# Optimization experiments

Hardware: AMD Instinct MI355X
Metric: run time of the kernel (lower is better)

Reference implementation:

```python
import jax, jax.numpy as jnp
import numpy as np
from jax import lax

BN_EPS = 1e-5

def setup_inputs() -> dict:
    key = jax.random.key(0)
    k1, k2, k3, k4 = jax.random.split(key, 4)
    B, Cin, Cout, H, Wd = 32, 256, 256, 56, 56
    x = jax.random.normal(k1, (B, Cin, H, Wd), dtype=jnp.float32)
    gate = jax.random.uniform(k2, (B, Cin), dtype=jnp.float32)
    # expert convs: one 3x3 conv per input channel; stacked into a full OIHW kernel
    W = jax.random.normal(k3, (Cout, Cin, 3, 3), dtype=jnp.float32) * (1.0 / np.sqrt(Cin * 9))
    # per-expert bias: expert i contributes gate[:, i] * b_expert[i]
    b_expert = jax.random.normal(k4, (Cin, Cout), dtype=jnp.float32) * 0.01
    gamma = jnp.ones((Cout,), dtype=jnp.float32)
    beta = jnp.zeros((Cout,), dtype=jnp.float32)
    return {"x": x, "gate": gate, "W": W, "b_expert": b_expert, "gamma": gamma, "beta": beta}

def reference(x, gate, W, b_expert, gamma, beta):
    # MoELayer: sum_i gate[:, i] * conv_i(x[:, i:i+1]) == conv2d(x * gate, W_full)
    xg = x * gate[:, :, None, None]
    y = lax.conv_general_dilated(
        xg, W, window_strides=(1, 1), padding=((1, 1), (1, 1)),
        dimension_numbers=("NCHW", "OIHW", "NCHW"))
    bias = jnp.einsum("bi,io->bo", gate, b_expert)  # gate-weighted expert biases
    y = y + bias[:, :, None, None]
    # BatchNorm2d (training mode: batch statistics over N,H,W) + ReLU
    mean = jnp.mean(y, axis=(0, 2, 3))
    var = jnp.var(y, axis=(0, 2, 3))
    inv = lax.rsqrt(var + BN_EPS)
    y = (y - mean[None, :, None, None]) * (inv * gamma)[None, :, None, None] + beta[None, :, None, None]
    return jax.nn.relu(y)
```

## Files before the change

kernel.cpp:

```cpp
#include <hip/hip_runtime.h>
#include <cstdint>
#include <cstddef>

#define S_IMG   3136
#define PPOS    3364
#define PLANE_B (PPOS * 16)
#define XPAD_BYTES (32 * 8 * 4 * PLANE_B)
#define WT2_OFF    XPAD_BYTES
#define WT2_BYTES  (9 * 8 * 4 * 256 * 16)
#define STATS_OFF  (WT2_OFF + WT2_BYTES)

typedef __bf16 bf16x8 __attribute__((ext_vector_type(8)));
typedef short  s16x8  __attribute__((ext_vector_type(8)));
typedef float  f32x4  __attribute__((ext_vector_type(4)));

__device__ __forceinline__ unsigned short f2bf(float f) {
    unsigned u = __float_as_uint(f);
    u += 0x7fffu + ((u >> 16) & 1u);
    return (unsigned short)(u >> 16);
}

__device__ __forceinline__ void gll16(const void* g, void* l) {
    __builtin_amdgcn_global_load_lds(
        (const __attribute__((address_space(1))) void*)g,
        (__attribute__((address_space(3))) void*)l, 16, 0, 0);
}

__global__ __launch_bounds__(256) void prep_small(const float* __restrict__ W,
                                                  const float* __restrict__ gate,
                                                  const float* __restrict__ be,
                                                  char* __restrict__ xpad,
                                                  char* __restrict__ wt2,
                                                  float* __restrict__ stats) {
    const int blk = blockIdx.x;
    if (blk < 917) {
        const int t = blk * 256 + threadIdx.x;
        if (t < 1024 * 228) {
            const int plane = t / 228, pi = t % 228;
            int pos;
            if (pi < 58)       pos = pi;
            else if (pi < 116) pos = 3306 + (pi - 58);
            else { const int q = pi - 116; pos = ((q >> 1) + 1) * 58 + (q & 1) * 57; }
            *(uint4*)(xpad + (size_t)plane * PLANE_B + (size_t)pos * 16) =
                make_uint4(0u, 0u, 0u, 0u);
        } else if (t < 1024 * 228 + 512) {
            stats[t - 1024 * 228] = 0.f;
        }
    } else if (blk < 1205) {
        const int g = (blk - 917) * 256 + threadIdx.x;
        if (g >= 9 * 256 * 32) return;
        const int ci8 = g % 32;
        const int co  = (g / 32) % 256;
        const int tap = g / (32 * 256);
        const float* src = W + ((size_t)co * 256 + ci8 * 8) * 9 + tap;
        unsigned short v[8];
#pragma unroll
        for (int j = 0; j < 8; ++j) v[j] = f2bf(src[j * 9]);
        uint4 o;
        o.x = (unsigned)v[0] | ((unsigned)v[1] << 16);
        o.y = (unsigned)v[2] | ((unsigned)v[3] << 16);
        o.z = (unsigned)v[4] | ((unsigned)v[5] << 16);
        o.w = (unsigned)v[6] | ((unsigned)v[7] << 16);
        *(uint4*)(wt2 + ((size_t)(tap * 32 + ci8) * 256 + co) * 16) = o;
    } else {
        const int b = blk - 1205, co = threadIdx.x;
        const float* gb = gate + b * 256;
        float s = 0.f;
        for (int ci = 0; ci < 256; ++ci) s += gb[ci] * be[ci * 256 + co];
        stats[512 + b * 256 + co] = s;
    }
}

__global__ __launch_bounds__(256) void prep_x(const float* __restrict__ x,
                                              const float* __restrict__ gate,
                                              char* __restrict__ xpad) {
    __shared__ unsigned short xb[14336];
    const int tid = threadIdx.x;
    const int b = blockIdx.x / 56, h = blockIdx.x % 56;
    const float* xbase = x + (size_t)b * 256 * S_IMG + h * 56;
    const float* gb = gate + b * 256;
#pragma unroll
    for (int i = 0; i < 14; ++i) {
        const int e4 = i * 1024 + tid * 4;
        const int ci = e4 / 56, w = e4 % 56;
        const float4 v = *(const float4*)(xbase + (size_t)ci * S_IMG + w);
        const float g = gb[ci];
        ushort4 o;
        o.x = f2bf(v.x * g); o.y = f2bf(v.y * g);
        o.z = f2bf(v.z * g); o.w = f2bf(v.w * g);
        *(ushort4*)(xb + e4) = o;
    }
    __syncthreads();
    char* dst_b = xpad + (size_t)b * 32 * PLANE_B + ((size_t)((h + 1) * 58 + 1)) * 16;
#pragma unroll
    for (int i = 0; i < 7; ++i) {
        const int c = i * 256 + tid;
        const int pw = c % 56, cg = c / 56;
        const unsigned short* src = xb + cg * 8 * 56 + pw;
        uint4 o;
        o.x = (unsigned)src[0]   | ((unsigned)src[56]  << 16);
        o.y = (unsigned)src[112] | ((unsigned)src[168] << 16);
        o.z = (unsigned)src[224] | ((unsigned)src[280] << 16);
        o.w = (unsigned)src[336] | ((unsigned)src[392] << 16);
        *(uint4*)(dst_b + (size_t)cg * PLANE_B + (size_t)pw * 16) = o;
    }
}

__global__ __launch_bounds__(256) void conv_mfma(
    const char* __restrict__ xpad, const char* __restrict__ wt2,
    const float* __restrict__ biasws, float* __restrict__ y,
    float* __restrict__ sums, float* __restrict__ sumsq) {
    __shared__ __align__(16) char smem[49152];
    const int tid = threadIdx.x;
    const int lane = tid & 63, wave = tid >> 6;
    const int wm = wave >> 1, wn = wave & 1;

    const int L = blockIdx.x;
    const int xcd = L & 7, j = L >> 3;
    const int p   = xcd * 100 + (j >> 1);
    const int co0 = (j & 1) * 128;
    const int b   = p / 25;
    const int s0  = (p % 25) * 128;

    int sA = s0 + lane;       if (sA > S_IMG - 1) sA = S_IMG - 1;
    int sB = s0 + 64 + lane;  if (sB > S_IMG - 1) sB = S_IMG - 1;
    const int pA = sA + 59 + 2 * (sA / 56);
    const int pB = sB + 59 + 2 * (sB / 56);

    const int a_off = ((lane >> 4) * 2048) + (wm * 64 + (lane & 15)) * 16;
    const int b_off = 8192 + ((lane >> 4) * 2048) + (wn * 64 + (lane & 15)) * 16;

    f32x4 acc[4][4] = {};

    const char* xbase = xpad + (size_t)(b * 32 + wave) * PLANE_B;

    auto stage = [&](int k, int bufidx) {
        const int cc = k / 9, tap = k - cc * 9;
        const int off = (tap / 3) * 58 + (tap % 3) - 59;
        char* abase = smem + bufidx * 16384 + wave * 2048;
        char* bbase = abase + 8192;
        const char* asrc = wt2 + (size_t)((tap * 8 + cc) * 4 + wave) * 4096;
        gll16(asrc + (co0 + lane) * 16,      abase);
        gll16(asrc + (co0 + 64 + lane) * 16, abase + 1024);
        const char* bsrc = xbase + (size_t)cc * 4 * PLANE_B;
        gll16(bsrc + (pA + off) * 16, bbase);
        gll16(bsrc + (pB + off) * 16, bbase + 1024);
    };

    stage(0, 0);
    stage(1, 1);

#pragma unroll 3
    for (int k = 0; k < 72; ++k) {
        if (k < 70) asm volatile("s_waitcnt vmcnt(4)" ::: "memory");
        else        asm volatile("s_waitcnt vmcnt(0)" ::: "memory");
        __builtin_amdgcn_sched_barrier(0);
        __builtin_amdgcn_s_barrier();
        __builtin_amdgcn_sched_barrier(0);
        if (k + 2 < 72) stage(k + 2, (k + 2) % 3);

        const char* base = smem + (k % 3) * 16384;
        s16x8 af[4], bfr[4];
#pragma unroll
        for (int m = 0; m < 4; ++m) af[m]  = *(const s16x8*)(base + a_off + m * 256);
#pragma unroll
        for (int n = 0; n < 4; ++n) bfr[n] = *(const s16x8*)(base + b_off + n * 256);
        __builtin_amdgcn_s_setprio(1);
#pragma unroll
        for (int m = 0; m < 4; ++m)
#pragma unroll
            for (int n = 0; n < 4; ++n)
                acc[m][n] = __builtin_amdgcn_mfma_f32_16x16x32_bf16(
                    __builtin_bit_cast(bf16x8, af[m]),
                    __builtin_bit_cast(bf16x8, bfr[n]),
                    acc[m][n], 0, 0, 0);
        __builtin_amdgcn_s_setprio(0);
    }

    const int row_l = lane >> 4, col_l = lane & 15;
#pragma unroll
    for (int m = 0; m < 4; ++m) {
#pragma unroll
        for (int r = 0; r < 4; ++r) {
            const int co = co0 + wm * 64 + m * 16 + row_l * 4 + r;
            const float bv = biasws[b * 256 + co];
            float lsum = 0.f, lsq = 0.f;
#pragma unroll
            for (int n = 0; n < 4; ++n) {
                const int s = s0 + wn * 64 + n * 16 + col_l;
                if (s < S_IMG) {
                    const float v = acc[m][n][r] + bv;
                    y[(size_t)(b * 256 + co) * S_IMG + s] = v;
                    lsum += v; lsq += v * v;
                }
            }
#pragma unroll
            for (int d = 1; d < 16; d <<= 1) {
                lsum += __shfl_xor(lsum, d, 64);
                lsq  += __shfl_xor(lsq,  d, 64);
            }
            if (col_l == 0) {
                atomicAdd(&sums[co],  lsum);
                atomicAdd(&sumsq[co], lsq);
            }
        }
    }
}

__global__ __launch_bounds__(256) void bn_apply(float* __restrict__ y,
                                                const float* __restrict__ sums,
                                                const float* __restrict__ sumsq,
                                                const float* __restrict__ gamma,
                                                const float* __restrict__ beta) {
    const size_t i = (size_t)blockIdx.x * 256 + threadIdx.x;
    const int co = (int)((i / 784) & 255);
    const float inv_n = 1.f / (float)(32 * S_IMG);
    const float mean = sums[co] * inv_n;
    const float var  = sumsq[co] * inv_n - mean * mean;
    const float sc   = gamma[co] * rsqrtf(var + 1e-5f);
    const float sh   = beta[co] - mean * sc;
    float4 v = ((const float4*)y)[i];
    v.x = fmaxf(v.x * sc + sh, 0.f);
    v.y = fmaxf(v.y * sc + sh, 0.f);
    v.z = fmaxf(v.z * sc + sh, 0.f);
    v.w = fmaxf(v.w * sc + sh, 0.f);
    ((float4*)y)[i] = v;
}

extern "C" void kernel_launch(void* const* d_in, const int* in_sizes, int n_in,
                              void* d_out, int out_size, void* d_ws, size_t ws_size,
                              hipStream_t stream) {
    const float* x     = (const float*)d_in[0];
    const float* gate  = (const float*)d_in[1];
    const float* W     = (const float*)d_in[2];
    const float* be    = (const float*)d_in[3];
    const float* gamma = (const float*)d_in[4];
    const float* beta  = (const float*)d_in[5];
    float* y  = (float*)d_out;
    char*  ws = (char*)d_ws;

    char* xpad = ws;
    char* wt2  = ws + WT2_OFF;
    float* stats = (float*)(ws + STATS_OFF);
    float* sums  = stats;
    float* sumsq = stats + 256;
    float* bias  = stats + 512;

    hipLaunchKernelGGL(prep_small, dim3(1237),  dim3(256), 0, stream,
                       W, gate, be, xpad, wt2, stats);
    hipLaunchKernelGGL(prep_x,     dim3(32*56), dim3(256), 0, stream, x, gate, xpad);
    hipLaunchKernelGGL(conv_mfma,  dim3(1600),  dim3(256), 0, stream,
                       xpad, wt2, bias, y, sums, sumsq);
    hipLaunchKernelGGL(bn_apply,   dim3(25088), dim3(256), 0, stream,
                       y, sums, sumsq, gamma, beta);
}
```

Before: 470.9 us.

## Enlarge conv tile to 256x256 with 8 waves, double-buffered K=64 stages

The conv kernel moves from 128x128 tiles with 4 waves to 256-channel by 256-pixel tiles with 8 waves and 128KB of dynamic LDS. Each stage is double-buffered over 64 input channels, and the MMA work is interleaved with staggered global-to-LDS loads across sub-phases. The bias add is taken out of the epilogue: per-image channel sums are accumulated, and a new bn_finalize kernel folds the bias analytically into the statistics and per-image shifts. This is meant to raise arithmetic intensity and cut redundant input reloads. In exchange it adds more barriers, runs at one block per CU with 392 blocks, and lets tiles span image boundaries.

```diff
diff --git a/kernel.cpp b/kernel.cpp
--- a/kernel.cpp
+++ b/kernel.cpp
@@ -33,7 +33,7 @@
                                                   char* __restrict__ wt2,
                                                   float* __restrict__ stats) {
     const int blk = blockIdx.x;
-    if (blk < 917) {
+    if (blk < 945) {
         const int t = blk * 256 + threadIdx.x;
         if (t < 1024 * 228) {
             const int plane = t / 228, pi = t % 228;
@@ -43,11 +43,11 @@
             else { const int q = pi - 116; pos = ((q >> 1) + 1) * 58 + (q & 1) * 57; }
             *(uint4*)(xpad + (size_t)plane * PLANE_B + (size_t)pos * 16) =
                 make_uint4(0u, 0u, 0u, 0u);
-        } else if (t < 1024 * 228 + 512) {
+        } else {
             stats[t - 1024 * 228] = 0.f;
         }
-    } else if (blk < 1205) {
-        const int g = (blk - 917) * 256 + threadIdx.x;
+    } else if (blk < 1233) {
+        const int g = (blk - 945) * 256 + threadIdx.x;
         if (g >= 9 * 256 * 32) return;
         const int ci8 = g % 32;
         const int co  = (g / 32) % 256;
@@ -63,11 +63,11 @@
         o.w = (unsigned)v[6] | ((unsigned)v[7] << 16);
         *(uint4*)(wt2 + ((size_t)(tap * 32 + ci8) * 256 + co) * 16) = o;
     } else {
-        const int b = blk - 1205, co = threadIdx.x;
+        const int b = blk - 1233, co = threadIdx.x;
         const float* gb = gate + b * 256;
         float s = 0.f;
         for (int ci = 0; ci < 256; ++ci) s += gb[ci] * be[ci * 256 + co];
-        stats[512 + b * 256 + co] = s;
+        stats[8448 + b * 256 + co] = s;
     }
 }
 
@@ -106,119 +106,231 @@
     }
 }
 
-__global__ __launch_bounds__(256) void conv_mfma(
+__global__ __launch_bounds__(512, 1) void conv_mfma(
     const char* __restrict__ xpad, const char* __restrict__ wt2,
-    const float* __restrict__ biasws, float* __restrict__ y,
-    float* __restrict__ sums, float* __restrict__ sumsq) {
-    __shared__ __align__(16) char smem[49152];
+    float* __restrict__ y, float* __restrict__ Sb, float* __restrict__ sumsq) {
+    extern __shared__ char smem[];
     const int tid = threadIdx.x;
-    const int lane = tid & 63, wave = tid >> 6;
-    const int wm = wave >> 1, wn = wave & 1;
+    const int lane = tid & 63, w = tid >> 6;
+    const int wm = w >> 2, wn = w & 3;
 
     const int L = blockIdx.x;
-    const int xcd = L & 7, j = L >> 3;
-    const int p   = xcd * 100 + (j >> 1);
-    const int co0 = (j & 1) * 128;
-    const int b   = p / 25;
-    const int s0  = (p % 25) * 128;
-
-    int sA = s0 + lane;       if (sA > S_IMG - 1) sA = S_IMG - 1;
-    int sB = s0 + 64 + lane;  if (sB > S_IMG - 1) sB = S_IMG - 1;
-    const int pA = sA + 59 + 2 * (sA / 56);
-    const int pB = sB + 59 + 2 * (sB / 56);
-
-    const int a_off = ((lane >> 4) * 2048) + (wm * 64 + (lane & 15)) * 16;
-    const int b_off = 8192 + ((lane >> 4) * 2048) + (wn * 64 + (lane & 15)) * 16;
-
-    f32x4 acc[4][4] = {};
-
-    const char* xbase = xpad + (size_t)(b * 32 + wave) * PLANE_B;
-
-    auto stage = [&](int k, int bufidx) {
-        const int cc = k / 9, tap = k - cc * 9;
-        const int off = (tap / 3) * 58 + (tap % 3) - 59;
-        char* abase = smem + bufidx * 16384 + wave * 2048;
-        char* bbase = abase + 8192;
-        const char* asrc = wt2 + (size_t)((tap * 8 + cc) * 4 + wave) * 4096;
-        gll16(asrc + (co0 + lane) * 16,      abase);
-        gll16(asrc + (co0 + 64 + lane) * 16, abase + 1024);
-        const char* bsrc = xbase + (size_t)cc * 4 * PLANE_B;
-        gll16(bsrc + (pA + off) * 16, bbase);
-        gll16(bsrc + (pB + off) * 16, bbase + 1024);
-    };
-
-    stage(0, 0);
-    stage(1, 1);
-
-#pragma unroll 3
-    for (int k = 0; k < 72; ++k) {
-        if (k < 70) asm volatile("s_waitcnt vmcnt(4)" ::: "memory");
-        else        asm volatile("s_waitcnt vmcnt(0)" ::: "memory");
-        __builtin_amdgcn_sched_barrier(0);
-        __builtin_amdgcn_s_barrier();
-        __builtin_amdgcn_sched_barrier(0);
-        if (k + 2 < 72) stage(k + 2, (k + 2) % 3);
-
-        const char* base = smem + (k % 3) * 16384;
+    const int s0 = ((L & 7) * 49 + (L >> 3)) * 256;
+
+    const int coA16 = ((((w & 3) << 6) + lane) << 4);
+    const int kA = w >> 2;
+    const int gs = s0 + ((w & 3) << 6) + lane;
+    const int bimg = gs / 3136, sp = gs % 3136;
+    const int ppad = sp + 59 + 2 * (sp / 56);
+    const char* xB_lo = xpad + (size_t)(bimg * 32 + kA) * PLANE_B + (size_t)ppad * 16;
+    const char* xB_hi = xB_lo + 2 * (size_t)PLANE_B;
+
+    const int aoff = ((lane >> 4) << 12) + ((wm * 128 + (lane & 15)) << 4);
+    const int boff = 32768 + ((lane >> 4) << 12) + ((wn * 64 + (lane & 15)) << 4);
+
+    f32x4 acc[8][4] = {};
+
+#define GLL(SRC, DSTOFF) gll16((const void*)(SRC), (void*)(bufW + (DSTOFF) + w * 1024))
+
+    {
+        char* bufW = smem;
+        const long xo0 = -944L;
+        const long xo1 = xo0 + 4L * PLANE_B;
+        GLL(wt2 + (size_t)kA * 4096 + coA16, 0);
+        GLL(wt2 + (size_t)(kA + 2) * 4096 + coA16, 8192);
+        GLL(xB_lo + xo0, 32768);
+        GLL(xB_hi + xo0, 40960);
+        GLL(wt2 + (size_t)(4 + kA) * 4096 + coA16, 16384);
+        GLL(wt2 + (size_t)(6 + kA) * 4096 + coA16, 24576);
+        GLL(xB_lo + xo1, 49152);
+        GLL(xB_hi + xo1, 57344);
+        asm volatile("s_waitcnt vmcnt(4)" ::: "memory");
+        __builtin_amdgcn_sched_barrier(0);
+        __builtin_amdgcn_s_barrier();
+    }
+
+    int tap = 0, cp = 0;
+    for (int t = 0; t < 36; ++t) {
+        const char* bR = smem + ((t & 1) << 16);
+        char* bufW = smem + (((t + 1) & 1) << 16);
+        int ntap = tap + 1, ncp = cp;
+        if (ntap == 9) { ntap = 0; ncp = cp + 1; }
+        const int  ntoff  = (ntap / 3) * 58 + (ntap % 3) - 59;
+        const long nwbase = (long)(ntap * 8 + ncp * 2) * 16384;
+        const long nxoff0 = (long)ncp * 8 * PLANE_B + (long)ntoff * 16;
+        const long nxoff1 = nxoff0 + 4L * PLANE_B;
+        const bool st = (t < 35);
+
         s16x8 af[4], bfr[4];
 #pragma unroll
-        for (int m = 0; m < 4; ++m) af[m]  = *(const s16x8*)(base + a_off + m * 256);
-#pragma unroll
-        for (int n = 0; n < 4; ++n) bfr[n] = *(const s16x8*)(base + b_off + n * 256);
+        for (int mi = 0; mi < 4; ++mi) af[mi]  = *(const s16x8*)(bR + aoff + mi * 256);
+#pragma unroll
+        for (int n = 0; n < 4; ++n)    bfr[n] = *(const s16x8*)(bR + boff + n * 256);
+        if (st) {
+            GLL(wt2 + nwbase + (size_t)kA * 4096 + coA16, 0);
+            GLL(wt2 + nwbase + (size_t)(kA + 2) * 4096 + coA16, 8192);
+        }
+        __builtin_amdgcn_s_barrier();
+        asm volatile("s_waitcnt lgkmcnt(0)" ::: "memory");
+        __builtin_amdgcn_sched_barrier(0);
         __builtin_amdgcn_s_setprio(1);
 #pragma unroll
-        for (int m = 0; m < 4; ++m)
+        for (int mi = 0; mi < 4; ++mi)
 #pragma unroll
             for (int n = 0; n < 4; ++n)
-                acc[m][n] = __builtin_amdgcn_mfma_f32_16x16x32_bf16(
-                    __builtin_bit_cast(bf16x8, af[m]),
-                    __builtin_bit_cast(bf16x8, bfr[n]),
-                    acc[m][n], 0, 0, 0);
+                acc[mi][n] = __builtin_amdgcn_mfma_f32_16x16x32_bf16(
+                    __builtin_bit_cast(bf16x8, af[mi]),
+                    __builtin_bit_cast(bf16x8, bfr[n]), acc[mi][n], 0, 0, 0);
         __builtin_amdgcn_s_setprio(0);
-    }
+        __builtin_amdgcn_s_barrier();
+#pragma unroll
+        for (int mi = 0; mi < 4; ++mi)
+            af[mi] = *(const s16x8*)(bR + aoff + 1024 + mi * 256);
+        if (st) {
+            GLL(xB_lo + nxoff0, 32768);
+            GLL(xB_hi + nxoff0, 40960);
+        }
+        __builtin_amdgcn_s_barrier();
+        asm volatile("s_waitcnt lgkmcnt(0)" ::: "memory");
+        __builtin_amdgcn_sched_barrier(0);
+        __builtin_amdgcn_s_setprio(1);
+#pragma unroll
+        for (int mi = 0; mi < 4; ++mi)
+#pragma unroll
+            for (int n = 0; n < 4; ++n)
+                acc[4 + mi][n] = __builtin_amdgcn_mfma_f32_16x16x32_bf16(
+                    __builtin_bit_cast(bf16x8, af[mi]),
+                    __builtin_bit_cast(bf16x8, bfr[n]), acc[4 + mi][n], 0, 0, 0);
+        __builtin_amdgcn_s_setprio(0);
+        if (st) { asm volatile("s_waitcnt vmcnt(4)" ::: "memory"); }
+        else    { asm volatile("s_waitcnt vmcnt(0)" ::: "memory"); }
+        __builtin_amdgcn_sched_barrier(0);
+        __builtin_amdgcn_s_barrier();
+#pragma unroll
+        for (int mi = 0; mi < 4; ++mi)
+            af[mi]  = *(const s16x8*)(bR + 16384 + aoff + mi * 256);
+#pragma unroll
+        for (int n = 0; n < 4; ++n)
+            bfr[n] = *(const s16x8*)(bR + 16384 + boff + n * 256);
+        if (st) {
+            GLL(wt2 + nwbase + (size_t)(4 + kA) * 4096 + coA16, 16384);
+            GLL(wt2 + nwbase + (size_t)(6 + kA) * 4096 + coA16, 24576);
+        }
+        __builtin_amdgcn_s_barrier();
+        asm volatile("s_waitcnt lgkmcnt(0)" ::: "memory");
+        __builtin_amdgcn_sched_barrier(0);
+        __builtin_amdgcn_s_setprio(1);
+#pragma unroll
+        for (int mi = 0; mi < 4; ++mi)
+#pragma unroll
+            for (int n = 0; n < 4; ++n)
+                acc[mi][n] = __builtin_amdgcn_mfma_f32_16x16x32_bf16(
+                    __builtin_bit_cast(bf16x8, af[mi]),
+                    __builtin_bit_cast(bf16x8, bfr[n]), acc[mi][n], 0, 0, 0);
+        __builtin_amdgcn_s_setprio(0);
+        __builtin_amdgcn_s_barrier();
+#pragma unroll
+        for (int mi = 0; mi < 4; ++mi)
+            af[mi] = *(const s16x8*)(bR + 16384 + aoff + 1024 + mi * 256);
+        if (st) {
+            GLL(xB_lo + nxoff1, 49152);
+            GLL(xB_hi + nxoff1, 57344);
+        }
+        __builtin_amdgcn_s_barrier();
+        asm volatile("s_waitcnt lgkmcnt(0)" ::: "memory");
+        __builtin_amdgcn_sched_barrier(0);
+        __builtin_amdgcn_s_setprio(1);
+#pragma unroll
+        for (int mi = 0; mi < 4; ++mi)
+#pragma unroll
+            for (int n = 0; n < 4; ++n)
+                acc[4 + mi][n] = __builtin_amdgcn_mfma_f32_16x16x32_bf16(
+                    __builtin_bit_cast(bf16x8, af[mi]),
+                    __builtin_bit_cast(bf16x8, bfr[n]), acc[4 + mi][n], 0, 0, 0);
+        __builtin_amdgcn_s_setprio(0);
+        asm volatile("s_waitcnt vmcnt(4)" ::: "memory");
+        __builtin_amdgcn_sched_barrier(0);
+        __builtin_amdgcn_s_barrier();
+        tap = ntap; cp = ncp;
+    }
+#undef GLL
 
     const int row_l = lane >> 4, col_l = lane & 15;
-#pragma unroll
-    for (int m = 0; m < 4; ++m) {
+    const int gbase = s0 + wn * 64 + col_l;
+    int bN[4]; size_t ybase[4];
+#pragma unroll
+    for (int n = 0; n < 4; ++n) {
+        const int g = gbase + n * 16;
+        const int bb = g / 3136, ss = g % 3136;
+        bN[n] = bb;
+        ybase[n] = (size_t)bb * 256 * 3136 + ss;
+    }
+    const int b0 = bN[0], b3 = bN[3];
+    const bool bsplit = (b3 != b0);
+    const int cobase = wm * 128 + row_l * 4;
+#pragma unroll
+    for (int m = 0; m < 8; ++m) {
 #pragma unroll
         for (int r = 0; r < 4; ++r) {
-            const int co = co0 + wm * 64 + m * 16 + row_l * 4 + r;
-            const float bv = biasws[b * 256 + co];
-            float lsum = 0.f, lsq = 0.f;
+            const int co = cobase + m * 16 + r;
+            float ls0 = 0.f, ls1 = 0.f, lq = 0.f;
 #pragma unroll
             for (int n = 0; n < 4; ++n) {
-                const int s = s0 + wn * 64 + n * 16 + col_l;
-                if (s < S_IMG) {
-                    const float v = acc[m][n][r] + bv;
-                    y[(size_t)(b * 256 + co) * S_IMG + s] = v;
-                    lsum += v; lsq += v * v;
-                }
+                const float v = acc[m][n][r];
+                y[ybase[n] + (size_t)co * 3136] = v;
+                lq += v * v;
+                if (bN[n] == b0) ls0 += v; else ls1 += v;
             }
 #pragma unroll
             for (int d = 1; d < 16; d <<= 1) {
-                lsum += __shfl_xor(lsum, d, 64);
-                lsq  += __shfl_xor(lsq,  d, 64);
+                ls0 += __shfl_xor(ls0, d, 64);
+                lq  += __shfl_xor(lq,  d, 64);
+            }
+            if (bsplit) {
+#pragma unroll
+                for (int d = 1; d < 16; d <<= 1) ls1 += __shfl_xor(ls1, d, 64);
             }
             if (col_l == 0) {
-                atomicAdd(&sums[co],  lsum);
-                atomicAdd(&sumsq[co], lsq);
+                atomicAdd(&Sb[b0 * 256 + co], ls0);
+                atomicAdd(&sumsq[co], lq);
+                if (bsplit) atomicAdd(&Sb[b3 * 256 + co], ls1);
             }
         }
     }
 }
 
+__global__ void bn_finalize(const float* __restrict__ stats,
+                            const float* __restrict__ gamma,
+                            const float* __restrict__ beta,
+                            float* __restrict__ scale,
+                            float* __restrict__ shiftb) {
+    const int co = threadIdx.x;
+    const float* Sb   = stats;
+    const float* ssq  = stats + 8192;
+    const float* bias = stats + 8448;
+    float tot = 0.f, tsq = ssq[co];
+#pragma unroll 4
+    for (int b = 0; b < 32; ++b) {
+        const float S = Sb[b * 256 + co], bb = bias[b * 256 + co];
+        tot += S + bb * 3136.f;
+        tsq += 2.f * bb * S + bb * bb * 3136.f;
+    }
+    const float inv_n = 1.f / 100352.f;
+    const float mean = tot * inv_n;
+    const float var  = tsq * inv_n - mean * mean;
+    const float sc   = gamma[co] * rsqrtf(var + 1e-5f);
+    scale[co] = sc;
+    const float bt = beta[co];
+    for (int b = 0; b < 32; ++b)
+        shiftb[b * 256 + co] = (bias[b * 256 + co] - mean) * sc + bt;
+}
+
 __global__ __launch_bounds__(256) void bn_apply(float* __restrict__ y,
-                                                const float* __restrict__ sums,
-                                                const float* __restrict__ sumsq,
-                                                const float* __restrict__ gamma,
-                                                const float* __restrict__ beta) {
+                                                const float* __restrict__ scale,
+                                                const float* __restrict__ shiftb) {
     const size_t i = (size_t)blockIdx.x * 256 + threadIdx.x;
-    const int co = (int)((i / 784) & 255);
-    const float inv_n = 1.f / (float)(32 * S_IMG);
-    const float mean = sums[co] * inv_n;
-    const float var  = sumsq[co] * inv_n - mean * mean;
-    const float sc   = gamma[co] * rsqrtf(var + 1e-5f);
-    const float sh   = beta[co] - mean * sc;
+    const int row = (int)(i / 784);
+    const float sc = scale[row & 255], sh = shiftb[row];
     float4 v = ((const float4*)y)[i];
     v.x = fmaxf(v.x * sc + sh, 0.f);
     v.y = fmaxf(v.y * sc + sh, 0.f);
@@ -239,18 +351,21 @@
     float* y  = (float*)d_out;
     char*  ws = (char*)d_ws;
 
-    char* xpad = ws;
-    char* wt2  = ws + WT2_OFF;
+    char*  xpad  = ws;
+    char*  wt2   = ws + WT2_OFF;
     float* stats = (float*)(ws + STATS_OFF);
-    float* sums  = stats;
-    float* sumsq = stats + 256;
-    float* bias  = stats + 512;
-
-    hipLaunchKernelGGL(prep_small, dim3(1237),  dim3(256), 0, stream,
+    float* Sb    = stats;
+    float* sumsq = stats + 8192;
+    float* scale = stats + 16640;
+    float* shiftb= stats + 16896;
+
+    hipLaunchKernelGGL(prep_small, dim3(1265),  dim3(256), 0, stream,
                        W, gate, be, xpad, wt2, stats);
     hipLaunchKernelGGL(prep_x,     dim3(32*56), dim3(256), 0, stream, x, gate, xpad);
-    hipLaunchKernelGGL(conv_mfma,  dim3(1600),  dim3(256), 0, stream,
-                       xpad, wt2, bias, y, sums, sumsq);
+    hipLaunchKernelGGL(conv_mfma,  dim3(392),   dim3(512), 131072, stream,
+                       xpad, wt2, y, Sb, sumsq);
+    hipLaunchKernelGGL(bn_finalize,dim3(1),     dim3(256), 0, stream,
+                       stats, gamma, beta, scale, shiftb);
     hipLaunchKernelGGL(bn_apply,   dim3(25088), dim3(256), 0, stream,
-                       y, sums, sumsq, gamma, beta);
-}
+                       y, scale, shiftb);
+}
```

Result: slower. 592.2 us (+25.8%).
